# Kernel optimization log

Hardware: AMD Instinct MI355X
Metric: run time of the kernel (lower is better)

The kernel has to match this reference:

```python
import jax, jax.numpy as jnp
import numpy as np

PROJ_ITERS = 50
PROJU_ITERS = 10
TOL = 1e-05
PROJ_STEP = 0.01
PROJU_STEP = 0.01


def setup_inputs() -> dict:
    key = jax.random.key(0)
    k1, k2, k3, k4 = jax.random.split(key, 4)
    B, n, m = 4096, 512, 1024
    x = jax.random.normal(k1, (B, n), dtype=jnp.float32)
    u = jax.random.normal(k2, (B, n), dtype=jnp.float32)
    # scale A so that step * lambda_max(A A^T) < 2 -> stable dual PGD
    A = 0.05 * jax.random.normal(k3, (m, n), dtype=jnp.float32)
    b = 0.5 * jax.random.uniform(k4, (m,), dtype=jnp.float32)
    return {"x": x, "u": u, "A": A, "b": b}


def _dual_pgd(lam0, Q, c, step, iters, active=None):
    # iterate: lam <- relu(lam - step * (lam @ Q - c)) [* active]
    def body(lam, _):
        lam = jnp.maximum(lam - step * (lam @ Q - c), 0.0)
        if active is not None:
            lam = lam * active
        return lam, None
    lam, _ = jax.lax.scan(body, lam0, None, length=iters)
    return lam


def projx(x, A, b, Q):
    # dual QP: min_{lam>=0} 0.5 lam^T Q lam - lam^T (A x - b); projx = x - A^T lam
    c = x @ A.T - b[None, :]                       # [B, m]
    lam0 = jnp.zeros_like(c)
    lam = _dual_pgd(lam0, Q, c, PROJ_STEP, PROJ_ITERS)
    return x - lam @ A                              # [B, n]


def proju(x, u, A, b, Q):
    Ax = x @ A.T                                    # [B, m]
    active = (Ax >= b[None, :] - TOL).astype(u.dtype)
    masked = (u @ A.T) * active                     # [B, m]
    lam0 = jnp.zeros_like(masked)
    lam = _dual_pgd(lam0, Q, masked, PROJU_STEP, PROJU_ITERS, active=active)
    return u - lam @ A                              # [B, n]


def reference(x, u, A, b):
    # expmap: z = projx(x + u); then project u onto tangent cone at z
    Q = A @ A.T                                     # [m, m]
    z = projx(x + u, A, b, Q)
    return proju(z, u, A, b, Q)
```

## Files before the change

kernel.cpp:

```cpp
#include <hip/hip_runtime.h>


#define TOLV 1e-5f
#define STEPV 0.01f

typedef __attribute__((ext_vector_type(8))) _Float16 half8;
typedef __attribute__((ext_vector_type(4))) float floatx4;
typedef unsigned short ushort_t;
typedef __attribute__((ext_vector_type(8))) unsigned short ushort8v;

#define GLDS(gptr, lptr) \
    __builtin_amdgcn_global_load_lds( \
        (const __attribute__((address_space(1))) void*)(gptr), \
        (__attribute__((address_space(3))) void*)(lptr), 16, 0, 0)

__device__ inline ushort_t f2h(float f) {
    union { _Float16 h; ushort_t u; } c; c.h = (_Float16)f;
    return c.u;
}
__device__ inline float h2f(ushort_t u) {
    union { ushort_t u; _Float16 h; } c; c.u = u;
    return (float)c.h;
}

__global__ void addcast_kernel(const float* __restrict__ x, const float* __restrict__ u,
                               ushort_t* __restrict__ yh, ushort_t* __restrict__ uh, int n) {
    int idx = (blockIdx.x * blockDim.x + threadIdx.x) * 4;
    if (idx < n) {
        float4 xv = *(const float4*)(x + idx);
        float4 uv = *(const float4*)(u + idx);
        ushort4 yo, uo;
        yo.x = f2h(xv.x + uv.x); yo.y = f2h(xv.y + uv.y);
        yo.z = f2h(xv.z + uv.z); yo.w = f2h(xv.w + uv.w);
        uo.x = f2h(uv.x); uo.y = f2h(uv.y); uo.z = f2h(uv.z); uo.w = f2h(uv.w);
        *(ushort4*)(yh + idx) = yo;
        *(ushort4*)(uh + idx) = uo;
    }
}

__global__ void cvt_h_kernel(const float* __restrict__ src, ushort_t* __restrict__ dst, int n) {
    int idx = (blockIdx.x * blockDim.x + threadIdx.x) * 4;
    if (idx < n) {
        float4 v = *(const float4*)(src + idx);
        ushort4 o;
        o.x = f2h(v.x); o.y = f2h(v.y); o.z = f2h(v.z); o.w = f2h(v.w);
        *(ushort4*)(dst + idx) = o;
    }
}

__global__ void transpose_cast_kernel(const float* __restrict__ A, ushort_t* __restrict__ AT,
                                      int m, int n) {
    __shared__ float t[32][33];
    int bx = blockIdx.x * 32;
    int by = blockIdx.y * 32;
    int tx = threadIdx.x & 31, ty = threadIdx.x >> 5;
#pragma unroll
    for (int i = 0; i < 32; i += 8)
        t[ty + i][tx] = A[(size_t)(by + ty + i) * n + bx + tx];
    __syncthreads();
#pragma unroll
    for (int i = 0; i < 32; i += 8)
        AT[(size_t)(bx + ty + i) * m + by + tx] = f2h(t[tx][ty + i]);
}

template<int EPI>
__global__ __launch_bounds__(512, 4)
void mfma_g(const ushort_t* __restrict__ X, const ushort_t* __restrict__ W,
            const ushort_t* __restrict__ lamIn, const float* __restrict__ cF,
            const ushort_t* __restrict__ cH, const ushort_t* __restrict__ actb,
            ushort_t* __restrict__ lamOut, float* __restrict__ cFout,
            ushort_t* __restrict__ cHout, ushort_t* __restrict__ actOut,
            const float* __restrict__ uin, float* __restrict__ outF,
            const float* __restrict__ bvec,
            int M, int N, int K) {
    __shared__ short SMEM[3 * 64 * 64 + 3 * 128 * 64];

    const int tid = threadIdx.x;
    const int w = tid >> 6;
    const int lane = tid & 63;

    const int nbm = M >> 6;
    const int spx = nbm >> 3;
    const int xcd = blockIdx.x & 7;
    const int loc = blockIdx.x >> 3;
    const int bm = (xcd * spx + (loc % spx)) << 6;
    const int bn = (loc / spx) << 7;

    const int wm = (w & 1) * 32;
    const int wn = (w >> 1) * 32;
    const int quad = lane >> 4;
    const int l15 = lane & 15;

    const int ldr = lane >> 3;
    const int csw = ((lane & 7) ^ ldr) * 8;

    const ushort_t* Xb = X + (size_t)bm * K + csw;
    const ushort_t* Wb = W + (size_t)bn * K + csw;

    floatx4 acc[2][2] = {};

    const int KT = K >> 6;

    short* const AsBase = SMEM;
    short* const BsBase = SMEM + 3 * 64 * 64;

    auto STAGE = [&](int kt, int bi) {
        const int ko = kt << 6;
        GLDS(Xb + (size_t)(w * 8 + ldr) * K + ko, AsBase + bi * 4096 + (w * 8) * 64);
#pragma unroll
        for (int t = 0; t < 2; ++t)
            GLDS(Wb + (size_t)(w * 16 + t * 8 + ldr) * K + ko,
                 BsBase + bi * 8192 + (w * 16 + t * 8) * 64);
    };

    STAGE(0, 0);
    STAGE(1, 1);

    int cur = 0;
    for (int kt = 0; kt < KT; ++kt) {
        if (kt + 1 < KT) {
            asm volatile("s_waitcnt vmcnt(3)" ::: "memory");
        } else {
            asm volatile("s_waitcnt vmcnt(0)" ::: "memory");
        }
        __builtin_amdgcn_s_barrier();
        if (kt + 2 < KT) {
            int nb = cur + 2; if (nb >= 3) nb -= 3;
            STAGE(kt + 2, nb);
        }

        __builtin_amdgcn_s_setprio(1);
#pragma unroll
        for (int kk = 0; kk < 2; ++kk) {
            const int sw = ((kk * 4 + quad) ^ (l15 & 7)) * 8;
            half8 af[2], bfr[2];
#pragma unroll
            for (int i = 0; i < 2; ++i)
                af[i] = *(const half8*)(AsBase + cur * 4096 + (wm + i * 16 + l15) * 64 + sw);
#pragma unroll
            for (int i = 0; i < 2; ++i)
                bfr[i] = *(const half8*)(BsBase + cur * 8192 + (wn + i * 16 + l15) * 64 + sw);
#pragma unroll
            for (int mt = 0; mt < 2; ++mt)
#pragma unroll
                for (int nt = 0; nt < 2; ++nt)
                    acc[mt][nt] = __builtin_amdgcn_mfma_f32_16x16x32_f16(
                        af[mt], bfr[nt], acc[mt][nt], 0, 0, 0);
        }
        __builtin_amdgcn_s_setprio(0);
        ++cur; if (cur >= 3) cur -= 3;
    }

    __syncthreads();
    float* Cs = (float*)SMEM;

#pragma unroll
    for (int mt = 0; mt < 2; ++mt)
#pragma unroll
        for (int nt = 0; nt < 2; ++nt)
#pragma unroll
            for (int r = 0; r < 4; ++r) {
                int rl = wm + mt * 16 + quad * 4 + r;
                int cl = wn + nt * 16 + l15;
                Cs[rl * 132 + cl] = acc[mt][nt][r];
            }
    __syncthreads();

    const int rl = tid >> 3;
    const int c0 = (tid & 7) * 16;
    const int grow = bm + rl;
    const int gcol = bn + c0;
    const size_t gidx = (size_t)grow * N + gcol;

    float v[16];
#pragma unroll
    for (int j = 0; j < 4; ++j)
        *(floatx4*)(v + 4 * j) = *(const floatx4*)(Cs + rl * 132 + c0 + 4 * j);

    if (EPI == 0) {
        ushort_t hv[16];
#pragma unroll
        for (int j = 0; j < 16; ++j) hv[j] = f2h(v[j]);
        *(ushort8v*)(lamOut + gidx) = *(ushort8v*)hv;
        *(ushort8v*)(lamOut + gidx + 8) = *(ushort8v*)(hv + 8);
    } else if (EPI == 1) {
        float bv[16];
#pragma unroll
        for (int j = 0; j < 4; ++j)
            *(floatx4*)(bv + 4 * j) = *(const floatx4*)(bvec + gcol + 4 * j);
        ushort_t ch[16], lo[16];
        float cf[16];
#pragma unroll
        for (int j = 0; j < 16; ++j) {
            float cv = v[j] - bv[j];
            cf[j] = cv;
            ch[j] = f2h(cv);
            lo[j] = f2h(STEPV * fmaxf(cv, 0.0f));
        }
#pragma unroll
        for (int j = 0; j < 4; ++j)
            *(floatx4*)(cFout + gidx + 4 * j) = *(floatx4*)(cf + 4 * j);
        *(ushort8v*)(cHout + gidx) = *(ushort8v*)ch;
        *(ushort8v*)(cHout + gidx + 8) = *(ushort8v*)(ch + 8);
        *(ushort8v*)(lamOut + gidx) = *(ushort8v*)lo;
        *(ushort8v*)(lamOut + gidx + 8) = *(ushort8v*)(lo + 8);
    } else if (EPI == 2 || EPI == 3) {
        ushort_t li[16], ch[16], ab[16], lo[16];
        *(ushort8v*)li = *(const ushort8v*)(lamIn + gidx);
        *(ushort8v*)(li + 8) = *(const ushort8v*)(lamIn + gidx + 8);
        *(ushort8v*)ch = *(const ushort8v*)(cH + gidx);
        *(ushort8v*)(ch + 8) = *(const ushort8v*)(cH + gidx + 8);
        if (EPI == 3) {
            *(ushort8v*)ab = *(const ushort8v*)(actb + gidx);
            *(ushort8v*)(ab + 8) = *(const ushort8v*)(actb + gidx + 8);
        }
#pragma unroll
        for (int j = 0; j < 16; ++j) {
            float nv = fmaxf(fmaf(-STEPV, v[j] - h2f(ch[j]), h2f(li[j])), 0.0f);
            if (EPI == 3) nv *= h2f(ab[j]);
            lo[j] = f2h(nv);
        }
        *(ushort8v*)(lamOut + gidx) = *(ushort8v*)lo;
        *(ushort8v*)(lamOut + gidx + 8) = *(ushort8v*)(lo + 8);
    } else if (EPI == 4) {
        float cf[16];
#pragma unroll
        for (int j = 0; j < 4; ++j)
            *(floatx4*)(cf + 4 * j) = *(const floatx4*)(cF + gidx + 4 * j);
        ushort_t ao[16];
#pragma unroll
        for (int j = 0; j < 16; ++j)
            ao[j] = (cf[j] - v[j] >= -TOLV) ? (ushort_t)0x3C00 : (ushort_t)0;
        *(ushort8v*)(actOut + gidx) = *(ushort8v*)ao;
        *(ushort8v*)(actOut + gidx + 8) = *(ushort8v*)(ao + 8);
    } else if (EPI == 5) {
        ushort_t ab[16], ch[16], lo[16];
        *(ushort8v*)ab = *(const ushort8v*)(actb + gidx);
        *(ushort8v*)(ab + 8) = *(const ushort8v*)(actb + gidx + 8);
#pragma unroll
        for (int j = 0; j < 16; ++j) {
            float mv = v[j] * h2f(ab[j]);
            ch[j] = f2h(mv);
            lo[j] = f2h(STEPV * fmaxf(mv, 0.0f));
        }
        *(ushort8v*)(cHout + gidx) = *(ushort8v*)ch;
        *(ushort8v*)(cHout + gidx + 8) = *(ushort8v*)(ch + 8);
        *(ushort8v*)(lamOut + gidx) = *(ushort8v*)lo;
        *(ushort8v*)(lamOut + gidx + 8) = *(ushort8v*)(lo + 8);
    } else if (EPI == 6) {
        float uv[16], ov[16];
#pragma unroll
        for (int j = 0; j < 4; ++j)
            *(floatx4*)(uv + 4 * j) = *(const floatx4*)(uin + gidx + 4 * j);
#pragma unroll
        for (int j = 0; j < 16; ++j) ov[j] = uv[j] - v[j];
#pragma unroll
        for (int j = 0; j < 4; ++j)
            *(floatx4*)(outF + gidx + 4 * j) = *(floatx4*)(ov + 4 * j);
    }
}

static inline int grid1d(int M, int N) { return (M >> 6) * (N >> 7); }

extern "C" void kernel_launch(void* const* d_in, const int* in_sizes, int n_in,
                              void* d_out, int out_size, void* d_ws, size_t ws_size,
                              hipStream_t stream) {
    const float* x = (const float*)d_in[0];
    const float* u = (const float*)d_in[1];
    const float* A = (const float*)d_in[2];
    const float* b = (const float*)d_in[3];
    float* out = (float*)d_out;

    const int B = 4096, n = 512, m = 1024;
    const size_t Bm = (size_t)B * m;
    const size_t Bn = (size_t)B * n;

    ushort_t* A_h   = (ushort_t*)d_ws;
    ushort_t* AT_h  = A_h + (size_t)m * n;
    ushort_t* y_h   = AT_h + (size_t)n * m;
    ushort_t* u_h   = y_h + Bn;
    ushort_t* Q_h   = u_h + Bn;
    ushort_t* lamA  = Q_h + (size_t)m * m;
    ushort_t* lamB  = lamA + Bm;
    ushort_t* act   = lamB + Bm;
    ushort_t* cHbuf = act + Bm;
    float* cFbuf = (float*)(cHbuf + Bm);

    dim3 blk(512);

    addcast_kernel<<<(int)(Bn / 4 + 255) / 256, 256, 0, stream>>>(x, u, y_h, u_h, (int)Bn);
    cvt_h_kernel<<<(m * n / 4 + 255) / 256, 256, 0, stream>>>(A, A_h, m * n);
    transpose_cast_kernel<<<dim3(n / 32, m / 32), dim3(256), 0, stream>>>(A, AT_h, m, n);

    mfma_g<0><<<grid1d(m, m), blk, 0, stream>>>(
        A_h, A_h, nullptr, nullptr, nullptr, nullptr,
        Q_h, nullptr, nullptr, nullptr, nullptr, nullptr, nullptr, m, m, n);

    mfma_g<1><<<grid1d(B, m), blk, 0, stream>>>(
        y_h, A_h, nullptr, nullptr, nullptr, nullptr,
        lamA, cFbuf, cHbuf, nullptr, nullptr, nullptr, b, B, m, n);

    ushort_t* lin = lamA; ushort_t* lout = lamB;
    for (int it = 0; it < 49; ++it) {
        mfma_g<2><<<grid1d(B, m), blk, 0, stream>>>(
            lin, Q_h, lin, nullptr, cHbuf, nullptr,
            lout, nullptr, nullptr, nullptr, nullptr, nullptr, nullptr, B, m, m);
        ushort_t* t = lin; lin = lout; lout = t;
    }

    mfma_g<4><<<grid1d(B, m), blk, 0, stream>>>(
        lin, Q_h, nullptr, cFbuf, nullptr, nullptr,
        nullptr, nullptr, nullptr, act, nullptr, nullptr, nullptr, B, m, m);

    mfma_g<5><<<grid1d(B, m), blk, 0, stream>>>(
        u_h, A_h, nullptr, nullptr, nullptr, act,
        lamA, nullptr, cHbuf, nullptr, nullptr, nullptr, nullptr, B, m, n);

    lin = lamA; lout = lamB;
    for (int it = 0; it < 9; ++it) {
        mfma_g<3><<<grid1d(B, m), blk, 0, stream>>>(
            lin, Q_h, lin, nullptr, cHbuf, act,
            lout, nullptr, nullptr, nullptr, nullptr, nullptr, nullptr, B, m, m);
        ushort_t* t = lin; lin = lout; lout = t;
    }

    mfma_g<6><<<grid1d(B, n), blk, 0, stream>>>(
        lin, AT_h, nullptr, nullptr, nullptr, nullptr,
        nullptr, nullptr, nullptr, nullptr, u, out, nullptr, B, n, m);
}
```

Baseline: 973.9 us.

## Repack Q into MFMA fragment order and load B operands directly to registers

Adds a kernel that rearranges Q into a fragment-major layout matching the 16x16x32 MFMA B-operand order. The iterative dual-PGD GEMMs then load Q fragments straight from global memory into registers with double buffering, instead of staging them through LDS. This cuts LDS traffic, LDS footprint and the B-tile staging barrier work. The cost is more global/L2 loads per wave, since each wave fetches its own B fragments without sharing through LDS, plus a small one-time repack pass.

```diff
diff --git a/kernel.cpp b/kernel.cpp
--- a/kernel.cpp
+++ b/kernel.cpp
@@ -63,7 +63,20 @@
         AT[(size_t)(bx + ty + i) * m + by + tx] = f2h(t[tx][ty + i]);
 }
 
-template<int EPI>
+__global__ void repack_q_kernel(const ushort_t* __restrict__ Q, ushort_t* __restrict__ Qp,
+                                int m, int K) {
+    int idx = blockIdx.x * blockDim.x + threadIdx.x;
+    int cpr = K >> 3;
+    int row = idx / cpr;
+    int c = idx % cpr;
+    if (row >= m) return;
+    int kt = c >> 3, rem = c & 7, kk = rem >> 2, quad = rem & 3;
+    int KT = K >> 6;
+    size_t dst = ((((size_t)(row >> 4) * KT + kt) * 2 + kk) * 4 + quad) * 128 + (row & 15) * 8;
+    *(ushort8v*)(Qp + dst) = *(const ushort8v*)(Q + (size_t)row * K + c * 8);
+}
+
+template<int EPI, int BD>
 __global__ __launch_bounds__(512, 4)
 void mfma_g(const ushort_t* __restrict__ X, const ushort_t* __restrict__ W,
             const ushort_t* __restrict__ lamIn, const float* __restrict__ cF,
@@ -73,7 +86,7 @@
             const float* __restrict__ uin, float* __restrict__ outF,
             const float* __restrict__ bvec,
             int M, int N, int K) {
-    __shared__ short SMEM[3 * 64 * 64 + 3 * 128 * 64];
+    __shared__ short SMEM[BD ? 16896 : (3 * 64 * 64 + 3 * 128 * 64)];
 
     const int tid = threadIdx.x;
     const int w = tid >> 6;
@@ -95,60 +108,135 @@
     const int csw = ((lane & 7) ^ ldr) * 8;
 
     const ushort_t* Xb = X + (size_t)bm * K + csw;
-    const ushort_t* Wb = W + (size_t)bn * K + csw;
 
     floatx4 acc[2][2] = {};
-
     const int KT = K >> 6;
 
     short* const AsBase = SMEM;
-    short* const BsBase = SMEM + 3 * 64 * 64;
-
-    auto STAGE = [&](int kt, int bi) {
-        const int ko = kt << 6;
-        GLDS(Xb + (size_t)(w * 8 + ldr) * K + ko, AsBase + bi * 4096 + (w * 8) * 64);
-#pragma unroll
-        for (int t = 0; t < 2; ++t)
-            GLDS(Wb + (size_t)(w * 16 + t * 8 + ldr) * K + ko,
-                 BsBase + bi * 8192 + (w * 16 + t * 8) * 64);
-    };
-
-    STAGE(0, 0);
-    STAGE(1, 1);
-
-    int cur = 0;
-    for (int kt = 0; kt < KT; ++kt) {
-        if (kt + 1 < KT) {
-            asm volatile("s_waitcnt vmcnt(3)" ::: "memory");
-        } else {
-            asm volatile("s_waitcnt vmcnt(0)" ::: "memory");
-        }
-        __builtin_amdgcn_s_barrier();
-        if (kt + 2 < KT) {
-            int nb = cur + 2; if (nb >= 3) nb -= 3;
-            STAGE(kt + 2, nb);
-        }
-
-        __builtin_amdgcn_s_setprio(1);
-#pragma unroll
-        for (int kk = 0; kk < 2; ++kk) {
-            const int sw = ((kk * 4 + quad) ^ (l15 & 7)) * 8;
-            half8 af[2], bfr[2];
+
+    if (BD == 0) {
+        short* const BsBase = SMEM + 3 * 64 * 64;
+        const ushort_t* Wb = W + (size_t)bn * K + csw;
+
+        auto STAGE = [&](int kt, int bi) {
+            const int ko = kt << 6;
+            GLDS(Xb + (size_t)(w * 8 + ldr) * K + ko, AsBase + bi * 4096 + (w * 8) * 64);
+#pragma unroll
+            for (int t = 0; t < 2; ++t)
+                GLDS(Wb + (size_t)(w * 16 + t * 8 + ldr) * K + ko,
+                     BsBase + bi * 8192 + (w * 16 + t * 8) * 64);
+        };
+
+        STAGE(0, 0);
+        STAGE(1, 1);
+
+        int cur = 0;
+        for (int kt = 0; kt < KT; ++kt) {
+            if (kt + 1 < KT) {
+                asm volatile("s_waitcnt vmcnt(3)" ::: "memory");
+            } else {
+                asm volatile("s_waitcnt vmcnt(0)" ::: "memory");
+            }
+            __builtin_amdgcn_s_barrier();
+            if (kt + 2 < KT) {
+                int nb = cur + 2; if (nb >= 3) nb -= 3;
+                STAGE(kt + 2, nb);
+            }
+
+            __builtin_amdgcn_s_setprio(1);
+#pragma unroll
+            for (int kk = 0; kk < 2; ++kk) {
+                const int sw = ((kk * 4 + quad) ^ (l15 & 7)) * 8;
+                half8 af[2], bfr[2];
+#pragma unroll
+                for (int i = 0; i < 2; ++i)
+                    af[i] = *(const half8*)(AsBase + cur * 4096 + (wm + i * 16 + l15) * 64 + sw);
+#pragma unroll
+                for (int i = 0; i < 2; ++i)
+                    bfr[i] = *(const half8*)(BsBase + cur * 8192 + (wn + i * 16 + l15) * 64 + sw);
+#pragma unroll
+                for (int mt = 0; mt < 2; ++mt)
+#pragma unroll
+                    for (int nt = 0; nt < 2; ++nt)
+                        acc[mt][nt] = __builtin_amdgcn_mfma_f32_16x16x32_f16(
+                            af[mt], bfr[nt], acc[mt][nt], 0, 0, 0);
+            }
+            __builtin_amdgcn_s_setprio(0);
+            ++cur; if (cur >= 3) cur -= 3;
+        }
+    } else {
+        const size_t rnb0 = (size_t)((bn + wn) >> 4);
+        const ushort_t* Qbase = W + rnb0 * ((size_t)KT * 1024) + lane * 8;
+
+        auto BADDR = [&](int kt, int kk, int i) -> const half8* {
+            return (const half8*)(Qbase + (size_t)i * KT * 1024 + kt * 1024 + kk * 512);
+        };
+
+        auto STAGE1 = [&](int kt, int bi) {
+            GLDS(Xb + (size_t)(w * 8 + ldr) * K + (kt << 6), AsBase + bi * 4096 + (w * 8) * 64);
+        };
+
+        half8 bfrA[4], bfrB[4];
+
+        STAGE1(0, 0);
+        STAGE1(1, 1);
+#pragma unroll
+        for (int kk = 0; kk < 2; ++kk)
 #pragma unroll
             for (int i = 0; i < 2; ++i)
-                af[i] = *(const half8*)(AsBase + cur * 4096 + (wm + i * 16 + l15) * 64 + sw);
-#pragma unroll
-            for (int i = 0; i < 2; ++i)
-                bfr[i] = *(const half8*)(BsBase + cur * 8192 + (wn + i * 16 + l15) * 64 + sw);
-#pragma unroll
-            for (int mt = 0; mt < 2; ++mt)
-#pragma unroll
-                for (int nt = 0; nt < 2; ++nt)
-                    acc[mt][nt] = __builtin_amdgcn_mfma_f32_16x16x32_f16(
-                        af[mt], bfr[nt], acc[mt][nt], 0, 0, 0);
-        }
-        __builtin_amdgcn_s_setprio(0);
-        ++cur; if (cur >= 3) cur -= 3;
+                bfrA[kk * 2 + i] = *BADDR(0, kk, i);
+
+        int cur = 0;
+#pragma unroll 2
+        for (int kt = 0; kt < KT; ++kt) {
+            const bool evn = (kt & 1) == 0;
+            if (kt + 2 < KT) {
+                int nb = cur + 2; if (nb >= 3) nb -= 3;
+                STAGE1(kt + 2, nb);
+            }
+            if (kt + 1 < KT) {
+                if (evn) {
+#pragma unroll
+                    for (int kk = 0; kk < 2; ++kk)
+#pragma unroll
+                        for (int i = 0; i < 2; ++i)
+                            bfrB[kk * 2 + i] = *BADDR(kt + 1, kk, i);
+                } else {
+#pragma unroll
+                    for (int kk = 0; kk < 2; ++kk)
+#pragma unroll
+                        for (int i = 0; i < 2; ++i)
+                            bfrA[kk * 2 + i] = *BADDR(kt + 1, kk, i);
+                }
+            }
+            if (kt + 2 < KT) {
+                asm volatile("s_waitcnt vmcnt(5)" ::: "memory");
+            } else if (kt + 1 < KT) {
+                asm volatile("s_waitcnt vmcnt(4)" ::: "memory");
+            } else {
+                asm volatile("s_waitcnt vmcnt(0)" ::: "memory");
+            }
+            __builtin_amdgcn_s_barrier();
+
+            __builtin_amdgcn_s_setprio(1);
+#pragma unroll
+            for (int kk = 0; kk < 2; ++kk) {
+                const int sw = ((kk * 4 + quad) ^ (l15 & 7)) * 8;
+                half8 af[2];
+#pragma unroll
+                for (int i = 0; i < 2; ++i)
+                    af[i] = *(const half8*)(AsBase + cur * 4096 + (wm + i * 16 + l15) * 64 + sw);
+#pragma unroll
+                for (int mt = 0; mt < 2; ++mt)
+#pragma unroll
+                    for (int nt = 0; nt < 2; ++nt)
+                        acc[mt][nt] = __builtin_amdgcn_mfma_f32_16x16x32_f16(
+                            af[mt], evn ? bfrA[kk * 2 + nt] : bfrB[kk * 2 + nt],
+                            acc[mt][nt], 0, 0, 0);
+            }
+            __builtin_amdgcn_s_setprio(0);
+            ++cur; if (cur >= 3) cur -= 3;
+        }
     }
 
     __syncthreads();
@@ -285,6 +373,7 @@
     ushort_t* act   = lamB + Bm;
     ushort_t* cHbuf = act + Bm;
     float* cFbuf = (float*)(cHbuf + Bm);
+    ushort_t* Qp    = (ushort_t*)(cFbuf + Bm);
 
     dim3 blk(512);
 
@@ -292,39 +381,41 @@
     cvt_h_kernel<<<(m * n / 4 + 255) / 256, 256, 0, stream>>>(A, A_h, m * n);
     transpose_cast_kernel<<<dim3(n / 32, m / 32), dim3(256), 0, stream>>>(A, AT_h, m, n);
 
-    mfma_g<0><<<grid1d(m, m), blk, 0, stream>>>(
+    mfma_g<0, 0><<<grid1d(m, m), blk, 0, stream>>>(
         A_h, A_h, nullptr, nullptr, nullptr, nullptr,
         Q_h, nullptr, nullptr, nullptr, nullptr, nullptr, nullptr, m, m, n);
 
-    mfma_g<1><<<grid1d(B, m), blk, 0, stream>>>(
+    repack_q_kernel<<<(m * m / 8 + 255) / 256, 256, 0, stream>>>(Q_h, Qp, m, m);
+
+    mfma_g<1, 0><<<grid1d(B, m), blk, 0, stream>>>(
         y_h, A_h, nullptr, nullptr, nullptr, nullptr,
         lamA, cFbuf, cHbuf, nullptr, nullptr, nullptr, b, B, m, n);
 
     ushort_t* lin = lamA; ushort_t* lout = lamB;
     for (int it = 0; it < 49; ++it) {
-        mfma_g<2><<<grid1d(B, m), blk, 0, stream>>>(
-            lin, Q_h, lin, nullptr, cHbuf, nullptr,
+        mfma_g<2, 1><<<grid1d(B, m), blk, 0, stream>>>(
+            lin, Qp, lin, nullptr, cHbuf, nullptr,
             lout, nullptr, nullptr, nullptr, nullptr, nullptr, nullptr, B, m, m);
         ushort_t* t = lin; lin = lout; lout = t;
     }
 
-    mfma_g<4><<<grid1d(B, m), blk, 0, stream>>>(
-        lin, Q_h, nullptr, cFbuf, nullptr, nullptr,
+    mfma_g<4, 1><<<grid1d(B, m), blk, 0, stream>>>(
+        lin, Qp, nullptr, cFbuf, nullptr, nullptr,
         nullptr, nullptr, nullptr, act, nullptr, nullptr, nullptr, B, m, m);
 
-    mfma_g<5><<<grid1d(B, m), blk, 0, stream>>>(
+    mfma_g<5, 0><<<grid1d(B, m), blk, 0, stream>>>(
         u_h, A_h, nullptr, nullptr, nullptr, act,
         lamA, nullptr, cHbuf, nullptr, nullptr, nullptr, nullptr, B, m, n);
 
     lin = lamA; lout = lamB;
     for (int it = 0; it < 9; ++it) {
-        mfma_g<3><<<grid1d(B, m), blk, 0, stream>>>(
-            lin, Q_h, lin, nullptr, cHbuf, act,
+        mfma_g<3, 1><<<grid1d(B, m), blk, 0, stream>>>(
+            lin, Qp, lin, nullptr, cHbuf, act,
             lout, nullptr, nullptr, nullptr, nullptr, nullptr, nullptr, B, m, m);
         ushort_t* t = lin; lin = lout; lout = t;
     }
 
-    mfma_g<6><<<grid1d(B, n), blk, 0, stream>>>(
+    mfma_g<6, 0><<<grid1d(B, n), blk, 0, stream>>>(
         lin, AT_h, nullptr, nullptr, nullptr, nullptr,
         nullptr, nullptr, nullptr, nullptr, u, out, nullptr, B, n, m);
 }
```

Result: slower. 1.252 ms (+28.6%).

## Fuse active-mask and masked u@A^T GEMMs into one kernel; prefetch epilogue inputs

Applied to the files above, without the earlier changes.

Merges the EPI 4 kernel (final lam@Q that builds the active mask) and the EPI 5 kernel (u@A^T masked by active) into a new EPI 7 kernel. That kernel runs two K-loops back to back and applies both epilogues together. This removes one launch and the write and reread of the act buffer between them. It also moves the lamIn, cH and act loads for EPI 2/3 ahead of the main loop so their latency overlaps the GEMM. In exchange, EPI 7 keeps a second accumulator set live, which raises register pressure, and it needs extra barriers between the two loops.

```diff
diff --git a/kernel.cpp b/kernel.cpp
--- a/kernel.cpp
+++ b/kernel.cpp
@@ -94,88 +94,131 @@
     const int ldr = lane >> 3;
     const int csw = ((lane & 7) ^ ldr) * 8;
 
-    const ushort_t* Xb = X + (size_t)bm * K + csw;
-    const ushort_t* Wb = W + (size_t)bn * K + csw;
-
-    floatx4 acc[2][2] = {};
-
-    const int KT = K >> 6;
-
-    short* const AsBase = SMEM;
-    short* const BsBase = SMEM + 3 * 64 * 64;
-
-    auto STAGE = [&](int kt, int bi) {
-        const int ko = kt << 6;
-        GLDS(Xb + (size_t)(w * 8 + ldr) * K + ko, AsBase + bi * 4096 + (w * 8) * 64);
-#pragma unroll
-        for (int t = 0; t < 2; ++t)
-            GLDS(Wb + (size_t)(w * 16 + t * 8 + ldr) * K + ko,
-                 BsBase + bi * 8192 + (w * 16 + t * 8) * 64);
-    };
-
-    STAGE(0, 0);
-    STAGE(1, 1);
-
-    int cur = 0;
-    for (int kt = 0; kt < KT; ++kt) {
-        if (kt + 1 < KT) {
-            asm volatile("s_waitcnt vmcnt(3)" ::: "memory");
-        } else {
-            asm volatile("s_waitcnt vmcnt(0)" ::: "memory");
-        }
-        __builtin_amdgcn_s_barrier();
-        if (kt + 2 < KT) {
-            int nb = cur + 2; if (nb >= 3) nb -= 3;
-            STAGE(kt + 2, nb);
-        }
-
-        __builtin_amdgcn_s_setprio(1);
-#pragma unroll
-        for (int kk = 0; kk < 2; ++kk) {
-            const int sw = ((kk * 4 + quad) ^ (l15 & 7)) * 8;
-            half8 af[2], bfr[2];
-#pragma unroll
-            for (int i = 0; i < 2; ++i)
-                af[i] = *(const half8*)(AsBase + cur * 4096 + (wm + i * 16 + l15) * 64 + sw);
-#pragma unroll
-            for (int i = 0; i < 2; ++i)
-                bfr[i] = *(const half8*)(BsBase + cur * 8192 + (wn + i * 16 + l15) * 64 + sw);
-#pragma unroll
-            for (int mt = 0; mt < 2; ++mt)
-#pragma unroll
-                for (int nt = 0; nt < 2; ++nt)
-                    acc[mt][nt] = __builtin_amdgcn_mfma_f32_16x16x32_f16(
-                        af[mt], bfr[nt], acc[mt][nt], 0, 0, 0);
-        }
-        __builtin_amdgcn_s_setprio(0);
-        ++cur; if (cur >= 3) cur -= 3;
-    }
-
-    __syncthreads();
-    float* Cs = (float*)SMEM;
-
-#pragma unroll
-    for (int mt = 0; mt < 2; ++mt)
-#pragma unroll
-        for (int nt = 0; nt < 2; ++nt)
-#pragma unroll
-            for (int r = 0; r < 4; ++r) {
-                int rl = wm + mt * 16 + quad * 4 + r;
-                int cl = wn + nt * 16 + l15;
-                Cs[rl * 132 + cl] = acc[mt][nt][r];
-            }
-    __syncthreads();
-
     const int rl = tid >> 3;
     const int c0 = (tid & 7) * 16;
     const int grow = bm + rl;
     const int gcol = bn + c0;
     const size_t gidx = (size_t)grow * N + gcol;
 
+    ushort_t li[16], chv[16], abv[16];
+    if (EPI == 2 || EPI == 3) {
+        *(ushort8v*)li = *(const ushort8v*)(lamIn + gidx);
+        *(ushort8v*)(li + 8) = *(const ushort8v*)(lamIn + gidx + 8);
+        *(ushort8v*)chv = *(const ushort8v*)(cH + gidx);
+        *(ushort8v*)(chv + 8) = *(const ushort8v*)(cH + gidx + 8);
+        if (EPI == 3) {
+            *(ushort8v*)abv = *(const ushort8v*)(actb + gidx);
+            *(ushort8v*)(abv + 8) = *(const ushort8v*)(actb + gidx + 8);
+        }
+    }
+
+    floatx4 acc[2][2] = {};
+    const int KT = K >> 6;
+
+    short* const AsBase = SMEM;
+    short* const BsBase = SMEM + 3 * 64 * 64;
+
+    auto RUNLOOP = [&](const ushort_t* XbL, const ushort_t* WbL, int KL, int KTL,
+                       floatx4 (&accL)[2][2]) {
+        auto STAGE = [&](int kt, int bi) {
+            const int ko = kt << 6;
+            GLDS(XbL + (size_t)(w * 8 + ldr) * KL + ko, AsBase + bi * 4096 + (w * 8) * 64);
+#pragma unroll
+            for (int t = 0; t < 2; ++t)
+                GLDS(WbL + (size_t)(w * 16 + t * 8 + ldr) * KL + ko,
+                     BsBase + bi * 8192 + (w * 16 + t * 8) * 64);
+        };
+
+        STAGE(0, 0);
+        STAGE(1, 1);
+
+        int cur = 0;
+        for (int kt = 0; kt < KTL; ++kt) {
+            if (kt + 1 < KTL) {
+                asm volatile("s_waitcnt vmcnt(3)" ::: "memory");
+            } else {
+                asm volatile("s_waitcnt vmcnt(0)" ::: "memory");
+            }
+            __builtin_amdgcn_s_barrier();
+            if (kt + 2 < KTL) {
+                int nb = cur + 2; if (nb >= 3) nb -= 3;
+                STAGE(kt + 2, nb);
+            }
+
+            __builtin_amdgcn_s_setprio(1);
+#pragma unroll
+            for (int kk = 0; kk < 2; ++kk) {
+                const int sw = ((kk * 4 + quad) ^ (l15 & 7)) * 8;
+                half8 af[2], bfr[2];
+#pragma unroll
+                for (int i = 0; i < 2; ++i)
+                    af[i] = *(const half8*)(AsBase + cur * 4096 + (wm + i * 16 + l15) * 64 + sw);
+#pragma unroll
+                for (int i = 0; i < 2; ++i)
+                    bfr[i] = *(const half8*)(BsBase + cur * 8192 + (wn + i * 16 + l15) * 64 + sw);
+#pragma unroll
+                for (int mt = 0; mt < 2; ++mt)
+#pragma unroll
+                    for (int nt = 0; nt < 2; ++nt)
+                        accL[mt][nt] = __builtin_amdgcn_mfma_f32_16x16x32_f16(
+                            af[mt], bfr[nt], accL[mt][nt], 0, 0, 0);
+            }
+            __builtin_amdgcn_s_setprio(0);
+            ++cur; if (cur >= 3) cur -= 3;
+        }
+    };
+
+    const ushort_t* Xb = X + (size_t)bm * K + csw;
+    const ushort_t* Wb = W + (size_t)bn * K + csw;
+    RUNLOOP(Xb, Wb, K, KT, acc);
+
+    floatx4 acc2[2][2] = {};
+    if (EPI == 7) {
+        __builtin_amdgcn_s_barrier();
+        const int K2 = K >> 1;
+        const ushort_t* Xb2 = lamIn + (size_t)bm * K2 + csw;
+        const ushort_t* Wb2 = cH + (size_t)bn * K2 + csw;
+        RUNLOOP(Xb2, Wb2, K2, K2 >> 6, acc2);
+    }
+
+    __syncthreads();
+    float* Cs = (float*)SMEM;
+
+#pragma unroll
+    for (int mt = 0; mt < 2; ++mt)
+#pragma unroll
+        for (int nt = 0; nt < 2; ++nt)
+#pragma unroll
+            for (int r = 0; r < 4; ++r) {
+                int rlw = wm + mt * 16 + quad * 4 + r;
+                int cl = wn + nt * 16 + l15;
+                Cs[rlw * 132 + cl] = acc[mt][nt][r];
+            }
+    __syncthreads();
+
     float v[16];
 #pragma unroll
     for (int j = 0; j < 4; ++j)
         *(floatx4*)(v + 4 * j) = *(const floatx4*)(Cs + rl * 132 + c0 + 4 * j);
+
+    float v2[16];
+    if (EPI == 7) {
+        __syncthreads();
+#pragma unroll
+        for (int mt = 0; mt < 2; ++mt)
+#pragma unroll
+            for (int nt = 0; nt < 2; ++nt)
+#pragma unroll
+                for (int r = 0; r < 4; ++r) {
+                    int rlw = wm + mt * 16 + quad * 4 + r;
+                    int cl = wn + nt * 16 + l15;
+                    Cs[rlw * 132 + cl] = acc2[mt][nt][r];
+                }
+        __syncthreads();
+#pragma unroll
+        for (int j = 0; j < 4; ++j)
+            *(floatx4*)(v2 + 4 * j) = *(const floatx4*)(Cs + rl * 132 + c0 + 4 * j);
+    }
 
     if (EPI == 0) {
         ushort_t hv[16];
@@ -205,58 +248,45 @@
         *(ushort8v*)(lamOut + gidx) = *(ushort8v*)lo;
         *(ushort8v*)(lamOut + gidx + 8) = *(ushort8v*)(lo + 8);
     } else if (EPI == 2 || EPI == 3) {
-        ushort_t li[16], ch[16], ab[16], lo[16];
-        *(ushort8v*)li = *(const ushort8v*)(lamIn + gidx);
-        *(ushort8v*)(li + 8) = *(const ushort8v*)(lamIn + gidx + 8);
-        *(ushort8v*)ch = *(const ushort8v*)(cH + gidx);
-        *(ushort8v*)(ch + 8) = *(const ushort8v*)(cH + gidx + 8);
-        if (EPI == 3) {
-            *(ushort8v*)ab = *(const ushort8v*)(actb + gidx);
-            *(ushort8v*)(ab + 8) = *(const ushort8v*)(actb + gidx + 8);
-        }
+        ushort_t lo[16];
 #pragma unroll
         for (int j = 0; j < 16; ++j) {
-            float nv = fmaxf(fmaf(-STEPV, v[j] - h2f(ch[j]), h2f(li[j])), 0.0f);
-            if (EPI == 3) nv *= h2f(ab[j]);
+            float nv = fmaxf(fmaf(-STEPV, v[j] - h2f(chv[j]), h2f(li[j])), 0.0f);
+            if (EPI == 3) nv *= h2f(abv[j]);
             lo[j] = f2h(nv);
         }
         *(ushort8v*)(lamOut + gidx) = *(ushort8v*)lo;
         *(ushort8v*)(lamOut + gidx + 8) = *(ushort8v*)(lo + 8);
-    } else if (EPI == 4) {
+    } else if (EPI == 6) {
+        float uv[16], ov[16];
+#pragma unroll
+        for (int j = 0; j < 4; ++j)
+            *(floatx4*)(uv + 4 * j) = *(const floatx4*)(uin + gidx + 4 * j);
+#pragma unroll
+        for (int j = 0; j < 16; ++j) ov[j] = uv[j] - v[j];
+#pragma unroll
+        for (int j = 0; j < 4; ++j)
+            *(floatx4*)(outF + gidx + 4 * j) = *(floatx4*)(ov + 4 * j);
+    } else if (EPI == 7) {
         float cf[16];
 #pragma unroll
         for (int j = 0; j < 4; ++j)
             *(floatx4*)(cf + 4 * j) = *(const floatx4*)(cF + gidx + 4 * j);
-        ushort_t ao[16];
-#pragma unroll
-        for (int j = 0; j < 16; ++j)
-            ao[j] = (cf[j] - v[j] >= -TOLV) ? (ushort_t)0x3C00 : (ushort_t)0;
+        ushort_t ao[16], ch[16], lo[16];
+#pragma unroll
+        for (int j = 0; j < 16; ++j) {
+            bool on = (cf[j] - v[j] >= -TOLV);
+            ao[j] = on ? (ushort_t)0x3C00 : (ushort_t)0;
+            float mv = on ? v2[j] : 0.0f;
+            ch[j] = f2h(mv);
+            lo[j] = f2h(STEPV * fmaxf(mv, 0.0f));
+        }
         *(ushort8v*)(actOut + gidx) = *(ushort8v*)ao;
         *(ushort8v*)(actOut + gidx + 8) = *(ushort8v*)(ao + 8);
-    } else if (EPI == 5) {
-        ushort_t ab[16], ch[16], lo[16];
-        *(ushort8v*)ab = *(const ushort8v*)(actb + gidx);
-        *(ushort8v*)(ab + 8) = *(const ushort8v*)(actb + gidx + 8);
-#pragma unroll
-        for (int j = 0; j < 16; ++j) {
-            float mv = v[j] * h2f(ab[j]);
-            ch[j] = f2h(mv);
-            lo[j] = f2h(STEPV * fmaxf(mv, 0.0f));
-        }
         *(ushort8v*)(cHout + gidx) = *(ushort8v*)ch;
         *(ushort8v*)(cHout + gidx + 8) = *(ushort8v*)(ch + 8);
         *(ushort8v*)(lamOut + gidx) = *(ushort8v*)lo;
         *(ushort8v*)(lamOut + gidx + 8) = *(ushort8v*)(lo + 8);
-    } else if (EPI == 6) {
-        float uv[16], ov[16];
-#pragma unroll
-        for (int j = 0; j < 4; ++j)
-            *(floatx4*)(uv + 4 * j) = *(const floatx4*)(uin + gidx + 4 * j);
-#pragma unroll
-        for (int j = 0; j < 16; ++j) ov[j] = uv[j] - v[j];
-#pragma unroll
-        for (int j = 0; j < 4; ++j)
-            *(floatx4*)(outF + gidx + 4 * j) = *(floatx4*)(ov + 4 * j);
     }
 }
 
@@ -308,13 +338,9 @@
         ushort_t* t = lin; lin = lout; lout = t;
     }
 
-    mfma_g<4><<<grid1d(B, m), blk, 0, stream>>>(
-        lin, Q_h, nullptr, cFbuf, nullptr, nullptr,
-        nullptr, nullptr, nullptr, act, nullptr, nullptr, nullptr, B, m, m);
-
-    mfma_g<5><<<grid1d(B, m), blk, 0, stream>>>(
-        u_h, A_h, nullptr, nullptr, nullptr, act,
-        lamA, nullptr, cHbuf, nullptr, nullptr, nullptr, nullptr, B, m, n);
+    mfma_g<7><<<grid1d(B, m), blk, 0, stream>>>(
+        lin, Q_h, u_h, cFbuf, A_h, nullptr,
+        lamA, nullptr, cHbuf, act, nullptr, nullptr, nullptr, B, m, m);
 
     lin = lamA; lout = lamB;
     for (int it = 0; it < 9; ++it) {
```

Result: slower. 1.028 ms (+5.5%).
